# Kernel tuning notes

Measured on AMD Instinct MI355X. Metric: run time of the kernel, lower is better.

The kernel has to match this reference:

```python
import jax, jax.numpy as jnp
import numpy as np

V, D, L = 128, 512, 4
B, S = 64, 1024
H = 2 * D          # LSTM hidden size
G = 4 * H          # gate dim (i,f,g,o)
RMS_EPS = 1.1920929e-07  # torch.finfo(float32).eps (nn.RMSNorm default eps=None)
LN_EPS = 1e-5


def setup_inputs() -> dict:
    key = jax.random.key(0)
    ks = jax.random.split(key, 8)
    sc = 1.0 / np.sqrt(H).astype(np.float32)
    return {
        "tokens": jax.random.randint(ks[0], (B, S), 0, V),
        "embedding": jax.random.normal(ks[1], (V, D), jnp.float32) * 0.02,
        "pre_norm_w": jnp.ones((L, D), jnp.float32),
        "W_ih": jax.random.normal(ks[2], (L, G, D), jnp.float32) * sc,
        "W_hh": jax.random.normal(ks[3], (L, G, H), jnp.float32) * sc,
        "b_ih": jnp.zeros((L, G), jnp.float32),
        "b_hh": jnp.zeros((L, G), jnp.float32),
        "W_out": jax.random.normal(ks[4], (L, D, H), jnp.float32) * sc,
        "b_out": jnp.zeros((L, D), jnp.float32),
        "ln_w": jnp.ones((L, D), jnp.float32),
        "ln_b": jnp.zeros((L, D), jnp.float32),
        "final_norm_w": jnp.ones((D,), jnp.float32),
        "head_W": jax.random.normal(ks[5], (V, D), jnp.float32) / np.sqrt(D),
        "head_b": jnp.zeros((V,), jnp.float32),
    }


def rmsnorm(x, w):
    var = jnp.mean(x * x, axis=-1, keepdims=True)
    return x * jax.lax.rsqrt(var + RMS_EPS) * w


def layernorm(x, w, b):
    mu = jnp.mean(x, axis=-1, keepdims=True)
    var = jnp.mean(jnp.square(x - mu), axis=-1, keepdims=True)
    return (x - mu) * jax.lax.rsqrt(var + LN_EPS) * w + b


def lstm(x, W_ih, W_hh, b_ih, b_hh):
    # x: [B,S,D] -> precompute input gates [S,B,4H], scan over time
    xg = jnp.einsum('bsd,gd->sbg', x, W_ih) + b_ih + b_hh
    bsz = x.shape[0]
    hdim = W_hh.shape[1]

    def step(carry, gx):
        h, c = carry
        g = gx + h @ W_hh.T
        i, f, gg, o = jnp.split(g, 4, axis=-1)
        c = jax.nn.sigmoid(f) * c + jax.nn.sigmoid(i) * jnp.tanh(gg)
        h = jax.nn.sigmoid(o) * jnp.tanh(c)
        return (h, c), h

    init = (jnp.zeros((bsz, hdim), x.dtype), jnp.zeros((bsz, hdim), x.dtype))
    _, hs = jax.lax.scan(step, init, xg)
    return hs.transpose(1, 0, 2)  # [B,S,H]


def reference(tokens, embedding, pre_norm_w, W_ih, W_hh, b_ih, b_hh,
              W_out, b_out, ln_w, ln_b, final_norm_w, head_W, head_b):
    x = embedding[tokens]  # [B,S,D]
    n_layers = pre_norm_w.shape[0]
    for l in range(n_layers):
        nx = rmsnorm(x, pre_norm_w[l])
        h = lstm(nx, W_ih[l], W_hh[l], b_ih[l], b_hh[l])
        out = jnp.einsum('bsh,dh->bsd', h, W_out[l]) + b_out[l]
        x = x + layernorm(out + nx, ln_w[l], ln_b[l])
    x = rmsnorm(x, final_norm_w)
    last = x[:, -1, :]                 # last token; dropout is identity (eval)
    return last @ head_W.T + head_b    # [B,V]
```

## Files before the change

### kernel.cpp

```cpp
#include <hip/hip_runtime.h>
#include <stdint.h>

typedef short bf16x8 __attribute__((ext_vector_type(8)));
typedef short s16x4  __attribute__((ext_vector_type(4)));
typedef float f32x4  __attribute__((ext_vector_type(4)));

__device__ __forceinline__ short f2bf(float f) {
  unsigned u = __builtin_bit_cast(unsigned, f);
  unsigned r = (u + 0x7fffu + ((u >> 16) & 1u)) >> 16;
  return (short)r;
}
__device__ __forceinline__ float bf2f(short s) {
  unsigned u = ((unsigned)(unsigned short)s) << 16;
  return __builtin_bit_cast(float, u);
}
__device__ __forceinline__ float sigf(float x) { return 1.f / (1.f + __expf(-x)); }
__device__ __forceinline__ float tanhf_(float x) {
  float e = __expf(2.f * x);
  return 1.f - 2.f / (e + 1.f);
}
__device__ __forceinline__ float wave_sum(float v) {
#pragma unroll
  for (int o = 32; o; o >>= 1) v += __shfl_xor(v, o, 64);
  return v;
}

__global__ void cvt_k(const float* __restrict__ a, short* __restrict__ o, int n) {
  int i = (blockIdx.x * 256 + threadIdx.x) * 4;
  if (i >= n) return;
  float4 v = *(const float4*)(a + i);
  s16x4 r;
  r[0] = f2bf(v.x); r[1] = f2bf(v.y); r[2] = f2bf(v.z); r[3] = f2bf(v.w);
  *(s16x4*)(o + i) = r;
}

__global__ void embed_k(const int* __restrict__ toks, const float* __restrict__ emb,
                        short* __restrict__ x) {
  const int t = blockIdx.x;
  const int tok = toks[t];
  const float4* src = (const float4*)(emb + (size_t)tok * 512);
  float4 a = src[threadIdx.x * 2], b = src[threadIdx.x * 2 + 1];
  bf16x8 o;
  o[0] = f2bf(a.x); o[1] = f2bf(a.y); o[2] = f2bf(a.z); o[3] = f2bf(a.w);
  o[4] = f2bf(b.x); o[5] = f2bf(b.y); o[6] = f2bf(b.z); o[7] = f2bf(b.w);
  *(bf16x8*)(x + (size_t)t * 512 + threadIdx.x * 8) = o;
}

__global__ void rms_k(const short* __restrict__ x, const float* __restrict__ w,
                      short* __restrict__ nx, int s0, int chsh, int chm) {
  const int t = blockIdx.x, b = t >> chsh, sl = t & chm;
  const short* xr = x + ((size_t)b * 1024 + s0 + sl) * 512;
  const int d0 = threadIdx.x * 8;
  bf16x8 xv = *(const bf16x8*)(xr + d0);
  float f[8];
  float ss = 0.f;
#pragma unroll
  for (int i = 0; i < 8; ++i) { f[i] = bf2f(xv[i]); ss += f[i] * f[i]; }
  ss = wave_sum(ss);
  float rs = rsqrtf(ss * (1.f / 512.f) + 1.1920929e-07f);
  float4 w0 = *(const float4*)(w + d0), w1 = *(const float4*)(w + d0 + 4);
  bf16x8 o;
  o[0] = f2bf(f[0] * rs * w0.x); o[1] = f2bf(f[1] * rs * w0.y);
  o[2] = f2bf(f[2] * rs * w0.z); o[3] = f2bf(f[3] * rs * w0.w);
  o[4] = f2bf(f[4] * rs * w1.x); o[5] = f2bf(f[5] * rs * w1.y);
  o[6] = f2bf(f[6] * rs * w1.z); o[7] = f2bf(f[7] * rs * w1.w);
  *(bf16x8*)(nx + (size_t)t * 512 + d0) = o;
}

template <int KD, int MODE>
__global__ __launch_bounds__(256, 2) void gemm_bt_k(
    const short* __restrict__ A, const short* __restrict__ Bw, short* __restrict__ Cb,
    const float* __restrict__ bias0, const float* __restrict__ bias1, int chsh, int chm) {
  __shared__ __align__(16) short lA[128 * 64];
  __shared__ __align__(16) short lB[128 * 64];
  const int tid = threadIdx.x, lane = tid & 63, wv = tid >> 6;
  const int wm = wv >> 1, wn = wv & 1;
  const int tm = blockIdx.x, tn = blockIdx.y;
  f32x4 acc[4][4] = {};
  const short* Abase = A + (size_t)tm * 128 * KD;
  const short* Bbase = Bw + (size_t)tn * 128 * KD;
  for (int k0 = 0; k0 < KD; k0 += 64) {
    __syncthreads();
#pragma unroll
    for (int i = 0; i < 4; ++i) {
      int e = i * 2048 + tid * 8;
      int row = e >> 6, c8 = (e >> 3) & 7;
      int dsto = row * 64 + ((c8 ^ (row & 7)) << 3);
      *(bf16x8*)(lA + dsto) = *(const bf16x8*)(Abase + (size_t)row * KD + k0 + (c8 << 3));
      *(bf16x8*)(lB + dsto) = *(const bf16x8*)(Bbase + (size_t)row * KD + k0 + (c8 << 3));
    }
    __syncthreads();
#pragma unroll
    for (int kk = 0; kk < 2; ++kk) {
      bf16x8 af[4], bfr[4];
#pragma unroll
      for (int i = 0; i < 4; ++i) {
        int ra = wm * 64 + i * 16 + (lane & 15);
        int rb = wn * 64 + i * 16 + (lane & 15);
        int k8 = kk * 4 + (lane >> 4);
        af[i] = *(const bf16x8*)(lA + ra * 64 + ((k8 ^ (ra & 7)) << 3));
        bfr[i] = *(const bf16x8*)(lB + rb * 64 + ((k8 ^ (rb & 7)) << 3));
      }
#pragma unroll
      for (int i = 0; i < 4; ++i)
#pragma unroll
        for (int j = 0; j < 4; ++j)
          acc[i][j] = __builtin_amdgcn_mfma_f32_16x16x32_bf16(af[i], bfr[j], acc[i][j], 0, 0, 0);
    }
  }
#pragma unroll
  for (int i = 0; i < 4; ++i) {
    int rbase = tm * 128 + wm * 64 + i * 16 + (lane >> 4) * 4;
#pragma unroll
    for (int j = 0; j < 4; ++j) {
      int col = tn * 128 + wn * 64 + j * 16 + (lane & 15);
      float badd = 0.f;
      if constexpr (MODE == 0) badd = bias0[col] + bias1[col];
#pragma unroll
      for (int r = 0; r < 4; ++r) {
        int rowi = rbase + r;
        float v = acc[i][j][r] + badd;
        if constexpr (MODE == 0) {
          int b = rowi >> chsh, sl = rowi & chm;
          Cb[((size_t)sl * 64 + b) * 4096 + col] = f2bf(v);
        } else {
          Cb[(size_t)rowi * 512 + col] = f2bf(v);
        }
      }
    }
  }
}

__global__ __launch_bounds__(256, 1) void lstm_rec_k(
    const short* __restrict__ xg,
    short* __restrict__ h_all,
    const short* __restrict__ Whh,
    short* __restrict__ h_buf,
    float* __restrict__ c_st,
    unsigned* __restrict__ bar, int step_base, int CH, int chsh) {
  const int tid = threadIdx.x, lane = tid & 63, wq = tid >> 6;
  const int grp = blockIdx.x >> 6, w = blockIdx.x & 63;
  const int j0 = w * 16, b0 = grp * 16;
  __shared__ __align__(16) short hstg[16384];
  __shared__ float gates[4][16][16];
  bf16x8 wf[32];
  {
    const short* wrow = Whh + (size_t)(wq * 1024 + j0 + (lane & 15)) * 1024 + (lane >> 4) * 8;
#pragma unroll
    for (int kt = 0; kt < 32; ++kt) wf[kt] = *(const bf16x8*)(wrow + kt * 32);
  }
  const int bb = tid >> 3, jj = (tid & 7) * 2;
  float c0 = 0.f, c1 = 0.f;
  if (tid < 128) {
    c0 = c_st[(size_t)(b0 + bb) * 1024 + j0 + jj];
    c1 = c_st[(size_t)(b0 + bb) * 1024 + j0 + jj + 1];
  }
  for (int s = 0; s < CH; ++s) {
    const int gstep = step_base + s;
    const short* hsrc = h_buf + (size_t)(gstep & 1) * 65536;
    short* hdst = h_buf + (size_t)((gstep + 1) & 1) * 65536;
#pragma unroll
    for (int it = 0; it < 8; ++it) {
      int si = it * 256 + tid;
      int kt = si >> 6, sl = si & 63;
      const short* gp = hsrc + (size_t)(b0 + (sl & 15)) * 1024 + kt * 32 + (sl >> 4) * 8;
      unsigned long long lo =
          __hip_atomic_load((const unsigned long long*)gp, __ATOMIC_RELAXED, __HIP_MEMORY_SCOPE_AGENT);
      unsigned long long hi = __hip_atomic_load((const unsigned long long*)(gp + 4),
                                                __ATOMIC_RELAXED, __HIP_MEMORY_SCOPE_AGENT);
      unsigned long long* dst = (unsigned long long*)(hstg) + (size_t)si * 2;
      dst[0] = lo; dst[1] = hi;
    }
    __syncthreads();
    f32x4 acc = {0.f, 0.f, 0.f, 0.f};
#pragma unroll
    for (int kt = 0; kt < 32; ++kt) {
      bf16x8 hf = *(const bf16x8*)(hstg + kt * 512 + lane * 8);
      acc = __builtin_amdgcn_mfma_f32_16x16x32_bf16(wf[kt], hf, acc, 0, 0, 0);
    }
#pragma unroll
    for (int r = 0; r < 4; ++r) gates[wq][lane & 15][(lane >> 4) * 4 + r] = acc[r];
    __syncthreads();
    if (tid < 128) {
      const short* xr = xg + ((size_t)s * 64 + b0 + bb) * 4096 + j0 + jj;
      float i0 = gates[0][bb][jj] + bf2f(xr[0]);
      float i1 = gates[0][bb][jj + 1] + bf2f(xr[1]);
      float f0 = gates[1][bb][jj] + bf2f(xr[1024]);
      float f1 = gates[1][bb][jj + 1] + bf2f(xr[1025]);
      float g0 = gates[2][bb][jj] + bf2f(xr[2048]);
      float g1 = gates[2][bb][jj + 1] + bf2f(xr[2049]);
      float o0 = gates[3][bb][jj] + bf2f(xr[3072]);
      float o1 = gates[3][bb][jj + 1] + bf2f(xr[3073]);
      c0 = sigf(f0) * c0 + sigf(i0) * tanhf_(g0);
      c1 = sigf(f1) * c1 + sigf(i1) * tanhf_(g1);
      float h0 = sigf(o0) * tanhf_(c0);
      float h1 = sigf(o1) * tanhf_(c1);
      unsigned pk = (unsigned)(unsigned short)f2bf(h0) |
                    (((unsigned)(unsigned short)f2bf(h1)) << 16);
      __hip_atomic_store((unsigned*)(hdst + (size_t)(b0 + bb) * 1024 + j0 + jj), pk,
                         __ATOMIC_RELAXED, __HIP_MEMORY_SCOPE_AGENT);
      *(unsigned*)(h_all + ((size_t)(((b0 + bb) << chsh) + s)) * 1024 + j0 + jj) = pk;
    }
    __syncthreads();
    if (tid == 0) {
      __hip_atomic_fetch_add(bar + grp * 64, 1u, __ATOMIC_RELAXED, __HIP_MEMORY_SCOPE_AGENT);
      const unsigned need = 64u * (unsigned)(gstep + 1);
      while (__hip_atomic_load(bar + grp * 64, __ATOMIC_RELAXED, __HIP_MEMORY_SCOPE_AGENT) < need)
        __builtin_amdgcn_s_sleep(1);
    }
    __syncthreads();
  }
  if (tid < 128) {
    c_st[(size_t)(b0 + bb) * 1024 + j0 + jj] = c0;
    c_st[(size_t)(b0 + bb) * 1024 + j0 + jj + 1] = c1;
  }
}

__global__ void ln_k(short* __restrict__ x, const short* __restrict__ outc,
                     const short* __restrict__ nxc, const float* __restrict__ bout,
                     const float* __restrict__ lnw, const float* __restrict__ lnb,
                     int s0, int chsh, int chm) {
  const int t = blockIdx.x, b = t >> chsh, sl = t & chm;
  short* xr = x + ((size_t)b * 1024 + s0 + sl) * 512;
  const int d0 = threadIdx.x * 8;
  bf16x8 ov = *(const bf16x8*)(outc + (size_t)t * 512 + d0);
  bf16x8 nv = *(const bf16x8*)(nxc + (size_t)t * 512 + d0);
  float v[8];
  float s = 0.f, ss = 0.f;
#pragma unroll
  for (int i = 0; i < 8; ++i) {
    v[i] = bf2f(ov[i]) + bout[d0 + i] + bf2f(nv[i]);
    s += v[i]; ss += v[i] * v[i];
  }
  s = wave_sum(s); ss = wave_sum(ss);
  float mu = s * (1.f / 512.f);
  float var = ss * (1.f / 512.f) - mu * mu;
  float rsd = rsqrtf(var + 1e-5f);
  bf16x8 xv = *(const bf16x8*)xr ? *(const bf16x8*)(xr + d0) : *(const bf16x8*)(xr + d0);
  xv = *(const bf16x8*)(xr + d0);
  bf16x8 o;
#pragma unroll
  for (int i = 0; i < 8; ++i)
    o[i] = f2bf(bf2f(xv[i]) + (v[i] - mu) * rsd * lnw[d0 + i] + lnb[d0 + i]);
  *(bf16x8*)(xr + d0) = o;
}

__global__ void head_k(const short* __restrict__ x, const float* __restrict__ fw,
                       const float* __restrict__ hW, const float* __restrict__ hb,
                       float* __restrict__ out) {
  const int b = blockIdx.x, v = threadIdx.x;
  __shared__ float xr[512];
  __shared__ float red[2];
  const short* row = x + ((size_t)b * 1024 + 1023) * 512;
  s16x4 xs = *(const s16x4*)(row + v * 4);
  float x0 = bf2f(xs[0]), x1 = bf2f(xs[1]), x2 = bf2f(xs[2]), x3 = bf2f(xs[3]);
  float ss = x0 * x0 + x1 * x1 + x2 * x2 + x3 * x3;
  ss = wave_sum(ss);
  if ((v & 63) == 0) red[v >> 6] = ss;
  __syncthreads();
  float rs = rsqrtf((red[0] + red[1]) * (1.f / 512.f) + 1.1920929e-07f);
  float4 fwv = *(const float4*)(fw + v * 4);
  xr[v * 4 + 0] = x0 * rs * fwv.x;
  xr[v * 4 + 1] = x1 * rs * fwv.y;
  xr[v * 4 + 2] = x2 * rs * fwv.z;
  xr[v * 4 + 3] = x3 * rs * fwv.w;
  __syncthreads();
  float a = hb[v];
  const float* wr = hW + (size_t)v * 512;
  for (int d = 0; d < 512; d += 4) {
    float4 w4 = *(const float4*)(wr + d);
    a += xr[d] * w4.x + xr[d + 1] * w4.y + xr[d + 2] * w4.z + xr[d + 3] * w4.w;
  }
  out[(size_t)b * 128 + v] = a;
}

extern "C" void kernel_launch(void* const* d_in, const int* in_sizes, int n_in,
                              void* d_out, int out_size, void* d_ws, size_t ws_size,
                              hipStream_t stream) {
  const int* toks = (const int*)d_in[0];
  const float* emb = (const float*)d_in[1];
  const float* prew = (const float*)d_in[2];
  const float* Wih = (const float*)d_in[3];
  const float* Whh = (const float*)d_in[4];
  const float* bih = (const float*)d_in[5];
  const float* bhh = (const float*)d_in[6];
  const float* Wout = (const float*)d_in[7];
  const float* bout = (const float*)d_in[8];
  const float* lnw = (const float*)d_in[9];
  const float* lnb = (const float*)d_in[10];
  const float* fnw = (const float*)d_in[11];
  const float* hW = (const float*)d_in[12];
  const float* hb = (const float*)d_in[13];
  (void)in_sizes; (void)n_in; (void)out_size;

  const size_t fixed = 4096 + 262144 + 262144
                     + (size_t)4096 * 512 * 2
                     + (size_t)4096 * 1024 * 2
                     + (size_t)512 * 1024 * 2
                     + (size_t)64 * 1024 * 512 * 2
                     + 16 * 256;
  int chsh = 5;
  for (int c = 8; c >= 5; --c) {
    size_t per = ((size_t)1 << c) * 720896;
    if (fixed + per <= ws_size) { chsh = c; break; }
  }
  const int CH = 1 << chsh, chm = CH - 1, chunks = 1024 >> chsh;

  char* w = (char*)d_ws;
  size_t off = 0;
  auto alloc = [&](size_t sz) {
    void* p = w + off;
    off = (off + sz + 255) & ~(size_t)255;
    return p;
  };
  unsigned* bar = (unsigned*)alloc(4096);
  short* h_buf = (short*)alloc(262144);
  float* c_st = (float*)alloc(262144);
  short* wihb = (short*)alloc((size_t)4096 * 512 * 2);
  short* whhb = (short*)alloc((size_t)4096 * 1024 * 2);
  short* woutb = (short*)alloc((size_t)512 * 1024 * 2);
  short* x = (short*)alloc((size_t)64 * 1024 * 512 * 2);
  short* nx = (short*)alloc((size_t)64 * CH * 512 * 2);
  short* hc = (short*)alloc((size_t)64 * CH * 1024 * 2);
  short* xgb = (short*)alloc((size_t)CH * 64 * 4096 * 2);
  short* outc = xgb;

  hipMemsetAsync(bar, 0, 4096, stream);
  embed_k<<<65536, 64, 0, stream>>>(toks, emb, x);

  for (int l = 0; l < 4; ++l) {
    hipMemsetAsync(h_buf, 0, 262144 + 262144, stream);
    cvt_k<<<2048, 256, 0, stream>>>(Wih + (size_t)l * 4096 * 512, wihb, 4096 * 512);
    cvt_k<<<4096, 256, 0, stream>>>(Whh + (size_t)l * 4096 * 1024, whhb, 4096 * 1024);
    cvt_k<<<512, 256, 0, stream>>>(Wout + (size_t)l * 512 * 1024, woutb, 512 * 1024);
    for (int ch = 0; ch < chunks; ++ch) {
      const int s0 = ch * CH;
      rms_k<<<64 * CH, 64, 0, stream>>>(x, prew + l * 512, nx, s0, chsh, chm);
      gemm_bt_k<512, 0><<<dim3(CH / 2, 32), 256, 0, stream>>>(
          nx, wihb, xgb, bih + l * 4096, bhh + l * 4096, chsh, chm);
      lstm_rec_k<<<256, 256, 0, stream>>>(xgb, hc, whhb, h_buf, c_st, bar,
                                          l * 1024 + s0, CH, chsh);
      gemm_bt_k<1024, 1><<<dim3(CH / 2, 4), 256, 0, stream>>>(
          hc, woutb, outc, nullptr, nullptr, chsh, chm);
      ln_k<<<64 * CH, 64, 0, stream>>>(x, outc, nx, bout + l * 512, lnw + l * 512,
                                       lnb + l * 512, s0, chsh, chm);
    }
  }
  head_k<<<64, 128, 0, stream>>>(x, fnw, hW, hb, (float*)d_out);
}
```

Measured before the change: 26.33 ms.

## Replace atomic counter barrier with per-block flags and prefetch MFMA-layout input gates

The recurrent LSTM kernel's group barrier changes from one shared atomic counter, polled by a single thread, to per-block step flags that one wave polls together with __all. This is meant to cut atomic contention and barrier latency on each timestep. The input-gate GEMM now writes xg in a layout that matches the MFMA accumulator fragment, so each lane prefetches its gate inputs for the next step and uses them to initialise the accumulator. The single accumulator chain is also split into four independent MFMA chains to shorten the dependency latency. A redundant load in the layernorm kernel is removed.

```diff
diff --git a/kernel.cpp b/kernel.cpp
--- a/kernel.cpp
+++ b/kernel.cpp
@@ -122,7 +122,10 @@
         float v = acc[i][j][r] + badd;
         if constexpr (MODE == 0) {
           int b = rowi >> chsh, sl = rowi & chm;
-          Cb[((size_t)sl * 64 + b) * 4096 + col] = f2bf(v);
+          size_t off = (size_t)sl * 262144 + (size_t)((col >> 4) & 63) * 4096 +
+                       (size_t)(b >> 4) * 1024 + (size_t)(col >> 10) * 256 +
+                       (size_t)(b & 15) * 16 + (size_t)(col & 15);
+          Cb[off] = f2bf(v);
         } else {
           Cb[(size_t)rowi * 512 + col] = f2bf(v);
         }
@@ -137,7 +140,8 @@
     const short* __restrict__ Whh,
     short* __restrict__ h_buf,
     float* __restrict__ c_st,
-    unsigned* __restrict__ bar, int step_base, int CH, int chsh) {
+    unsigned* __restrict__ flags,
+    int step_base, int CH, int chsh) {
   const int tid = threadIdx.x, lane = tid & 63, wq = tid >> 6;
   const int grp = blockIdx.x >> 6, w = blockIdx.x & 63;
   const int j0 = w * 16, b0 = grp * 16;
@@ -155,8 +159,12 @@
     c0 = c_st[(size_t)(b0 + bb) * 1024 + j0 + jj];
     c1 = c_st[(size_t)(b0 + bb) * 1024 + j0 + jj + 1];
   }
+  const short* xgl = xg + (size_t)(w * 4 + grp) * 1024 + wq * 256 +
+                     (size_t)(lane & 15) * 16 + (lane >> 4) * 4;
+  s16x4 cur = *(const s16x4*)xgl;
   for (int s = 0; s < CH; ++s) {
     const int gstep = step_base + s;
+    const unsigned need = (unsigned)(gstep + 1);
     const short* hsrc = h_buf + (size_t)(gstep & 1) * 65536;
     short* hdst = h_buf + (size_t)((gstep + 1) & 1) * 65536;
 #pragma unroll
@@ -172,25 +180,29 @@
       dst[0] = lo; dst[1] = hi;
     }
     __syncthreads();
-    f32x4 acc = {0.f, 0.f, 0.f, 0.f};
-#pragma unroll
-    for (int kt = 0; kt < 32; ++kt) {
-      bf16x8 hf = *(const bf16x8*)(hstg + kt * 512 + lane * 8);
-      acc = __builtin_amdgcn_mfma_f32_16x16x32_bf16(wf[kt], hf, acc, 0, 0, 0);
-    }
+    f32x4 a0, a1 = {0.f, 0.f, 0.f, 0.f}, a2 = {0.f, 0.f, 0.f, 0.f}, a3 = {0.f, 0.f, 0.f, 0.f};
+#pragma unroll
+    for (int r = 0; r < 4; ++r) a0[r] = bf2f(cur[r]);
+#pragma unroll
+    for (int kt = 0; kt < 32; kt += 4) {
+      a0 = __builtin_amdgcn_mfma_f32_16x16x32_bf16(
+          wf[kt], *(const bf16x8*)(hstg + kt * 512 + lane * 8), a0, 0, 0, 0);
+      a1 = __builtin_amdgcn_mfma_f32_16x16x32_bf16(
+          wf[kt + 1], *(const bf16x8*)(hstg + (kt + 1) * 512 + lane * 8), a1, 0, 0, 0);
+      a2 = __builtin_amdgcn_mfma_f32_16x16x32_bf16(
+          wf[kt + 2], *(const bf16x8*)(hstg + (kt + 2) * 512 + lane * 8), a2, 0, 0, 0);
+      a3 = __builtin_amdgcn_mfma_f32_16x16x32_bf16(
+          wf[kt + 3], *(const bf16x8*)(hstg + (kt + 3) * 512 + lane * 8), a3, 0, 0, 0);
+    }
+    f32x4 acc = (a0 + a1) + (a2 + a3);
 #pragma unroll
     for (int r = 0; r < 4; ++r) gates[wq][lane & 15][(lane >> 4) * 4 + r] = acc[r];
     __syncthreads();
     if (tid < 128) {
-      const short* xr = xg + ((size_t)s * 64 + b0 + bb) * 4096 + j0 + jj;
-      float i0 = gates[0][bb][jj] + bf2f(xr[0]);
-      float i1 = gates[0][bb][jj + 1] + bf2f(xr[1]);
-      float f0 = gates[1][bb][jj] + bf2f(xr[1024]);
-      float f1 = gates[1][bb][jj + 1] + bf2f(xr[1025]);
-      float g0 = gates[2][bb][jj] + bf2f(xr[2048]);
-      float g1 = gates[2][bb][jj + 1] + bf2f(xr[2049]);
-      float o0 = gates[3][bb][jj] + bf2f(xr[3072]);
-      float o1 = gates[3][bb][jj + 1] + bf2f(xr[3073]);
+      float i0 = gates[0][bb][jj],     i1 = gates[0][bb][jj + 1];
+      float f0 = gates[1][bb][jj],     f1 = gates[1][bb][jj + 1];
+      float g0 = gates[2][bb][jj],     g1 = gates[2][bb][jj + 1];
+      float o0 = gates[3][bb][jj],     o1 = gates[3][bb][jj + 1];
       c0 = sigf(f0) * c0 + sigf(i0) * tanhf_(g0);
       c1 = sigf(f1) * c1 + sigf(i1) * tanhf_(g1);
       float h0 = sigf(o0) * tanhf_(c0);
@@ -201,12 +213,17 @@
                          __ATOMIC_RELAXED, __HIP_MEMORY_SCOPE_AGENT);
       *(unsigned*)(h_all + ((size_t)(((b0 + bb) << chsh) + s)) * 1024 + j0 + jj) = pk;
     }
-    __syncthreads();
-    if (tid == 0) {
-      __hip_atomic_fetch_add(bar + grp * 64, 1u, __ATOMIC_RELAXED, __HIP_MEMORY_SCOPE_AGENT);
-      const unsigned need = 64u * (unsigned)(gstep + 1);
-      while (__hip_atomic_load(bar + grp * 64, __ATOMIC_RELAXED, __HIP_MEMORY_SCOPE_AGENT) < need)
-        __builtin_amdgcn_s_sleep(1);
+    if (s + 1 < CH) cur = *(const s16x4*)(xgl + (size_t)(s + 1) * 262144);
+    __syncthreads();
+    if (tid < 64) {
+      if (tid == 0)
+        __hip_atomic_store(flags + grp * 64 + w, need, __ATOMIC_RELAXED, __HIP_MEMORY_SCOPE_AGENT);
+      while (true) {
+        unsigned v = __hip_atomic_load(flags + grp * 64 + tid, __ATOMIC_RELAXED,
+                                       __HIP_MEMORY_SCOPE_AGENT);
+        if (__all(v >= need)) break;
+        __builtin_amdgcn_s_sleep(2);
+      }
     }
     __syncthreads();
   }
@@ -236,8 +253,7 @@
   float mu = s * (1.f / 512.f);
   float var = ss * (1.f / 512.f) - mu * mu;
   float rsd = rsqrtf(var + 1e-5f);
-  bf16x8 xv = *(const bf16x8*)xr ? *(const bf16x8*)(xr + d0) : *(const bf16x8*)(xr + d0);
-  xv = *(const bf16x8*)(xr + d0);
+  bf16x8 xv = *(const bf16x8*)(xr + d0);
   bf16x8 o;
 #pragma unroll
   for (int i = 0; i < 8; ++i)
@@ -313,7 +329,7 @@
     off = (off + sz + 255) & ~(size_t)255;
     return p;
   };
-  unsigned* bar = (unsigned*)alloc(4096);
+  unsigned* flags = (unsigned*)alloc(4096);
   short* h_buf = (short*)alloc(262144);
   float* c_st = (float*)alloc(262144);
   short* wihb = (short*)alloc((size_t)4096 * 512 * 2);
@@ -325,7 +341,7 @@
   short* xgb = (short*)alloc((size_t)CH * 64 * 4096 * 2);
   short* outc = xgb;
 
-  hipMemsetAsync(bar, 0, 4096, stream);
+  hipMemsetAsync(flags, 0, 4096, stream);
   embed_k<<<65536, 64, 0, stream>>>(toks, emb, x);
 
   for (int l = 0; l < 4; ++l) {
@@ -338,7 +354,7 @@
       rms_k<<<64 * CH, 64, 0, stream>>>(x, prew + l * 512, nx, s0, chsh, chm);
       gemm_bt_k<512, 0><<<dim3(CH / 2, 32), 256, 0, stream>>>(
           nx, wihb, xgb, bih + l * 4096, bhh + l * 4096, chsh, chm);
-      lstm_rec_k<<<256, 256, 0, stream>>>(xgb, hc, whhb, h_buf, c_st, bar,
+      lstm_rec_k<<<256, 256, 0, stream>>>(xgb, hc, whhb, h_buf, c_st, flags,
                                           l * 1024 + s0, CH, chsh);
       gemm_bt_k<1024, 1><<<dim3(CH / 2, 4), 256, 0, stream>>>(
           hc, woutb, outc, nullptr, nullptr, chsh, chm);
```

New measurement: 31.29 ms. 18.8% more time.
